# Optimization experiments

Measured on AMD Instinct MI355X. Metric: run time of the kernel, lower is better.

The kernel has to match this reference:

```python
import jax, jax.numpy as jnp
import numpy as np

B, T = 64, 2048
HID, FAST, SLOW, VOCAB = 256, 64, 256, 64
WRITE_THRESH = 0.4
NEG = -1000000000.0


def setup_inputs() -> dict:
    key = jax.random.key(0)
    ks = jax.random.split(key, 10)
    s = 0.05  # small init so gate sigmoids are not saturated
    return {
        "seq": jax.random.randint(ks[0], (B, T), 0, VOCAB),
        "emb": jax.random.normal(ks[1], (VOCAB, HID), jnp.float32),        # encoder embedding table
        "Wg": jax.random.normal(ks[2], (HID, 1), jnp.float32) * s,         # write_gate
        "bg": jnp.zeros((1,), jnp.float32),
        "Wd": jax.random.normal(ks[3], (HID, 1), jnp.float32) * s,         # demotion_net
        "bd": jnp.zeros((1,), jnp.float32),
        "Wq": jax.random.normal(ks[4], (HID, HID), jnp.float32) * s,       # read_head.q_proj
        "bq": jnp.zeros((HID,), jnp.float32),
        "Wo": jax.random.normal(ks[5], (HID, VOCAB), jnp.float32) * s,     # read_head.out
        "bo": jnp.zeros((VOCAB,), jnp.float32),
    }


def _process_sequence(h, Wg, bg, Wd, bd):
    # h: (B, T, H). Sequential LRU tiered-memory scatter, vectorized over batch.
    Bb, Tt, H = h.shape

    def step(state, tok_h):
        fm, sm, fa, sa, fu, su = state
        ws = jax.nn.sigmoid(tok_h @ Wg + bg)[:, 0]          # (B,) write score
        act = ws >= WRITE_THRESH                            # skip rows with score < 0.4
        fa = fa + fu.astype(jnp.int32)                      # age occupied slots
        sa = sa + su.astype(jnp.int32)
        free = ~fu
        has_free = jnp.any(free, axis=1)                    # (B,)
        free_idx = jnp.argmax(free, axis=1)                 # first free fast slot
        dem = ((fm @ Wd)[..., 0] + bd[0])                   # (B, FAST) demotion scores
        dem_slot = jnp.argmin(dem, axis=1)
        fslot = jnp.where(has_free, free_idx, dem_slot)     # fast slot to write
        foh = jax.nn.one_hot(fslot, FAST, dtype=bool)
        wf = act[:, None] & foh                              # (B, FAST) fast-write mask
        # value demoted to slow (only used when fast was full)
        demoted = jnp.take_along_axis(fm, fslot[:, None, None], axis=1)[:, 0, :]
        slow_act = act & ~has_free
        sfree = ~su
        s_has_free = jnp.any(sfree, axis=1)
        ss = jnp.where(s_has_free, jnp.argmax(sfree, axis=1), jnp.argmax(sa, axis=1))
        soh = jax.nn.one_hot(ss, SLOW, dtype=bool)
        wsm = slow_act[:, None] & soh                        # (B, SLOW) slow-write mask
        sm = jnp.where(wsm[..., None], demoted[:, None, :], sm)
        sa = jnp.where(wsm, 0, sa)
        su = su | wsm
        tok = jax.lax.stop_gradient(tok_h)                   # original writes tok_h.detach()
        fm = jnp.where(wf[..., None], tok[:, None, :], fm)
        fa = jnp.where(wf, 0, fa)
        fu = fu | wf
        return (fm, sm, fa, sa, fu, su), None

    init = (
        jnp.zeros((Bb, FAST, H), h.dtype),
        jnp.zeros((Bb, SLOW, H), h.dtype),
        jnp.zeros((Bb, FAST), jnp.int32),
        jnp.zeros((Bb, SLOW), jnp.int32),
        jnp.zeros((Bb, FAST), bool),
        jnp.zeros((Bb, SLOW), bool),
    )
    hs = jnp.swapaxes(h[:, : Tt - 3], 0, 1)                  # loop runs for T-3 tokens
    (fm, sm, fa, sa, fu, su), _ = jax.lax.scan(step, init, hs)
    memory = jnp.concatenate([fm, sm], axis=1)               # (B, F+S, H)
    mask = jnp.concatenate([fu, su], axis=1).astype(h.dtype)
    slow_mask = su.astype(h.dtype)
    return memory, mask, slow_mask


def reference(seq, emb, Wg, bg, Wd, bd, Wq, bq, Wo, bo):
    h = emb[seq]                                             # encoder: (B, T, H)
    memory, mask, slow_mask = _process_sequence(h, Wg, bg, Wd, bd)
    # ReadHead
    q = h[:, -1, :] @ Wq + bq                                # (B, H)
    scores = jnp.einsum("bnh,bh->bn", memory, q)
    scores = jnp.where(mask == 0, NEG, scores)
    attn = jax.nn.softmax(scores, axis=-1)
    ctx = jnp.einsum("bn,bnh->bh", attn, memory)
    logits = ctx @ Wo + bo                                   # (B, VOCAB)
    return logits, slow_mask
```

## Files before the change

kernel.cpp:

```cpp
#include <hip/hip_runtime.h>
#include <math.h>

#define BB 64
#define TT 2048
#define HIDD 256
#define FASTN 64
#define SLOWN 256
#define VOC 64
#define TLOOP (TT - 3)
#define NEGC -1000000000.0f
#define EPAD 257
#define NEGBIG (-(1 << 20))
#define BYTEAT(U, J) ((int)(((U) >> (8 * (J))) & 0xFFu))

__global__ __launch_bounds__(512) void k_one(
    const int* __restrict__ seq, const float* __restrict__ emb,
    const float* __restrict__ Wg, const float* __restrict__ bg,
    const float* __restrict__ Wd, const float* __restrict__ bd,
    const float* __restrict__ Wq, const float* __restrict__ bq,
    const float* __restrict__ Wo, const float* __restrict__ bo,
    float* __restrict__ out) {
  const int b = blockIdx.x;
  const int tid = threadIdx.x;
  const int lane = tid & 63;
  const int wv = tid >> 6;

  __shared__ float embS[VOC * EPAD];
  __shared__ __align__(16) unsigned char zsB[2080];
  __shared__ float qLastS[HIDD], ctxS[HIDD];
  __shared__ float pp[4][64];
  __shared__ float gp8[8][64], dp8[8][64];
  __shared__ float wS[64];
  __shared__ int prS[64], invS[64], cntTok[64];
  __shared__ int CS[4];
  __shared__ int PsS[4][64], QsS[4][64], aEndS[4][64], eSS[4][64];

  const int4* seq4 = (const int4*)(seq + b * TT);
  int4 sqa = make_int4(0, 0, 0, 0), sqb = make_int4(0, 0, 0, 0);
  if (tid < 256) { sqa = seq4[2 * tid]; sqb = seq4[2 * tid + 1]; }
  const int lastv = seq[b * TT + TT - 1];

  const float4* emb4 = (const float4*)emb;
  for (int i = tid; i < VOC * 64; i += 512) {
    float4 e = emb4[i];
    float* d = &embS[(i >> 6) * EPAD + ((i & 63) << 2)];
    d[0] = e.x; d[1] = e.y; d[2] = e.z; d[3] = e.w;
  }
  __syncthreads();

  {
    const int v = tid & 63, kp = tid >> 6;
    const float* er = &embS[v * EPAD + kp * 32];
    const float* wg = &Wg[kp * 32];
    const float* wd = &Wd[kp * 32];
    float g = 0.f, d = 0.f;
#pragma unroll 8
    for (int k = 0; k < 32; ++k) { float e = er[k]; g += e * wg[k]; d += e * wd[k]; }
    gp8[kp][v] = g; dp8[kp][v] = d;
  }
  __syncthreads();

  float qacc = 0.f;
  if (tid < 64) {
    float g = bg[0], dv = bd[0];
#pragma unroll
    for (int p = 0; p < 8; ++p) { g += gp8[p][tid]; dv += dp8[p][tid]; }
    int act = (1.f / (1.f + expf(-g)) >= 0.4f) ? 1 : 0;
    int r = 0;
#pragma unroll
    for (int s = 1; s < 64; ++s) {
      float du = __shfl_xor(dv, s);
      int u = lane ^ s;
      r += (du < dv || (du == dv && u < lane)) ? 1 : 0;
    }
    invS[r] = tid;
    prS[tid] = act ? r : 0xFF;
  } else if (tid >= 256) {
    const int j = tid - 256;
    const float* eL = &embS[lastv * EPAD];
#pragma unroll 8
    for (int k = 0; k < 128; ++k) qacc += eL[k] * Wq[k * HIDD + j];
  }
  __syncthreads();

  int by[8], cAct = 0, incl = 0;
  if (tid < 256) {
    const int t0 = tid * 8;
    int tk[8] = {sqa.x, sqa.y, sqa.z, sqa.w, sqb.x, sqb.y, sqb.z, sqb.w};
#pragma unroll
    for (int j = 0; j < 8; ++j) {
      int r = prS[tk[j]];
      by[j] = (t0 + j < TLOOP) ? r : 0xFF;
      cAct += (by[j] != 0xFF) ? 1 : 0;
    }
    incl = cAct;
    for (int s = 1; s < 64; s <<= 1) {
      int t = __shfl_up(incl, s);
      if (lane >= s) incl += t;
    }
    if (lane == 63) CS[wv] = incl;
  } else {
    const int j = tid - 256;
    const float* eL = &embS[lastv * EPAD];
#pragma unroll 8
    for (int k = 128; k < 256; ++k) qacc += eL[k] * Wq[k * HIDD + j];
    qLastS[j] = qacc + bq[j];
  }
  __syncthreads();

  const int A = CS[0] + CS[1] + CS[2] + CS[3];
  const int fsplit = A < 64 ? A : 64;
  const int nL = A - fsplit;
  const int win = nL < 256 ? nL : 256;
  const int wstart = A - win;
  const int L = (((A + 3) >> 2) + 15) & ~15;

  if (tid < 256) {
    int Ow = 0;
#pragma unroll
    for (int w2 = 0; w2 < 4; ++w2) Ow += (w2 < wv) ? CS[w2] : 0;
    int pos = Ow + incl - cAct;
#pragma unroll
    for (int j = 0; j < 8; ++j)
      if (by[j] != 0xFF) zsB[pos++] = (unsigned char)by[j];
  } else {
    const int j = tid - 256;
    out[BB * VOC + b * SLOWN + j] = (j < win) ? 1.0f : 0.0f;
  }
  __syncthreads();

  if (tid < 256) {
    const int baseW = wv * L;
    const int endW = min(baseW + L, A);
    int P = 0, Q = NEGBIG;
    for (int g = baseW; g < endW; g += 16) {
      uint4 t4 = *(const uint4*)(zsB + g);
      unsigned dsw[4] = {t4.x, t4.y, t4.z, t4.w};
      const int gHi = min(g + 16, endW);
      if (gHi == g + 16 && gHi <= fsplit) {
#pragma unroll
        for (int d = 0; d < 4; ++d)
#pragma unroll
          for (int j = 0; j < 4; ++j) {
            int x = (BYTEAT(dsw[d], j) <= lane) ? 1 : 0;
            P += x; Q += x;
          }
      } else if (gHi == g + 16 && g >= fsplit) {
#pragma unroll
        for (int d = 0; d < 4; ++d)
#pragma unroll
          for (int j = 0; j < 4; ++j) {
            int x = (BYTEAT(dsw[d], j) <= lane) ? 1 : 0;
            P += x - 1;
            Q = max(Q + x - 1, x);
          }
      } else {
#pragma unroll
        for (int d = 0; d < 4; ++d)
#pragma unroll
          for (int j = 0; j < 4; ++j) {
            int i = g + d * 4 + j;
            int x = (BYTEAT(dsw[d], j) <= lane) ? 1 : 0;
            bool vld = i < endW;
            bool fil = i < fsplit;
            int p = fil ? x : x - 1;
            int q = fil ? NEGBIG : x;
            int Pn = P + p;
            int Qn = max(Q + p, q);
            P = vld ? Pn : P;
            Q = vld ? Qn : Q;
          }
      }
    }
    PsS[wv][lane] = P;
    QsS[wv][lane] = Q;
  } else {
    const int v = tid & 63, part = wv - 4;
    const float* er = &embS[v * EPAD + part * 64];
    const float* qr = &qLastS[part * 64];
    float s = 0.f;
#pragma unroll 8
    for (int k = 0; k < 64; ++k) s += er[k] * qr[k];
    pp[part][v] = s;
  }
  __syncthreads();

  if (tid < 256) {
    int a = 0;
    for (int w2 = 0; w2 < wv; ++w2)
      a = max(a + PsS[w2][lane], QsS[w2][lane]);
    int e = 0;
    const int baseW = wv * L;
    const int endW = min(baseW + L, A);
    for (int g = baseW; g < endW; g += 16) {
      uint4 t4 = *(const uint4*)(zsB + g);
      unsigned dsw[4] = {t4.x, t4.y, t4.z, t4.w};
      const int gHi = min(g + 16, endW);
      const bool full = (gHi == g + 16);
      if (full && gHi <= fsplit) {
#pragma unroll
        for (int d = 0; d < 4; ++d)
#pragma unroll
          for (int j = 0; j < 4; ++j)
            a += (BYTEAT(dsw[d], j) <= lane) ? 1 : 0;
      } else if (full && g >= fsplit && gHi <= wstart) {
#pragma unroll
        for (int d = 0; d < 4; ++d)
#pragma unroll
          for (int j = 0; j < 4; ++j) {
            int xm1 = (BYTEAT(dsw[d], j) <= lane) ? 0 : -1;
            a = max(a, 1) + xm1;
          }
      } else if (full && g >= wstart) {
#pragma unroll
        for (int d = 0; d < 4; ++d)
#pragma unroll
          for (int j = 0; j < 4; ++j) {
            int xm1 = (BYTEAT(dsw[d], j) <= lane) ? 0 : -1;
            e += (a > 0) ? 1 : 0;
            a = max(a, 1) + xm1;
          }
      } else {
#pragma unroll
        for (int d = 0; d < 4; ++d)
#pragma unroll
          for (int j = 0; j < 4; ++j) {
            int i = g + d * 4 + j;
            int x = (BYTEAT(dsw[d], j) <= lane) ? 1 : 0;
            bool vld = i < endW;
            bool fil = i < fsplit;
            bool wg = vld && (i >= wstart);
            e += (wg && a > 0) ? 1 : 0;
            int af = a + x;
            int al = max(a, 1) + (x - 1);
            int an = fil ? af : al;
            a = vld ? an : a;
          }
      }
    }
    aEndS[wv][lane] = a;
    eSS[wv][lane] = e;
  }
  __syncthreads();

  if (tid < 64) {
    int af = aEndS[3][lane];
    int et = eSS[0][lane] + eSS[1][lane] + eSS[2][lane] + eSS[3][lane];
    int ap = __shfl_up(af, 1); if (lane == 0) ap = 0;
    int ep = __shfl_up(et, 1); if (lane == 0) ep = 0;
    cntTok[invS[lane]] = (af - ap) + (et - ep);
    float sc = pp[0][tid] + pp[1][tid] + pp[2][tid] + pp[3][tid];
    int cc = cntTok[tid];
    float m = (cc > 0) ? sc : NEGC;
    for (int off = 32; off; off >>= 1) m = fmaxf(m, __shfl_xor(m, off));
    float w = (cc > 0) ? (float)cc * expf(sc - m) : 0.f;
    float z = w;
    for (int off = 32; off; off >>= 1) z += __shfl_xor(z, off);
    z += (float)(FASTN + SLOWN - (fsplit + win)) * expf(NEGC - m);
    wS[tid] = w / z;
  }
  __syncthreads();

  if (tid < 256) {
    float cacc = 0.f;
#pragma unroll 8
    for (int u = 0; u < 64; ++u) cacc += wS[u] * embS[u * EPAD + tid];
    ctxS[tid] = cacc;
  }
  __syncthreads();

  if (tid < 256) {
    const int o = tid & 63, part = tid >> 6;
    const float* cr = &ctxS[part * 64];
    const float* wr = &Wo[part * 64 * VOC + o];
    float s = 0.f;
#pragma unroll 8
    for (int k = 0; k < 64; ++k) s += cr[k] * wr[k * VOC];
    pp[part][o] = s;
  }
  __syncthreads();
  if (tid < 64)
    out[b * VOC + tid] = pp[0][tid] + pp[1][tid] + pp[2][tid] + pp[3][tid] + bo[tid];
}

extern "C" void kernel_launch(void* const* d_in, const int* in_sizes, int n_in,
                              void* d_out, int out_size, void* d_ws, size_t ws_size,
                              hipStream_t stream) {
  const int*   seq = (const int*)d_in[0];
  const float* emb = (const float*)d_in[1];
  const float* Wg  = (const float*)d_in[2];
  const float* bg  = (const float*)d_in[3];
  const float* Wd  = (const float*)d_in[4];
  const float* bd  = (const float*)d_in[5];
  const float* Wq  = (const float*)d_in[6];
  const float* bq  = (const float*)d_in[7];
  const float* Wo  = (const float*)d_in[8];
  const float* bo  = (const float*)d_in[9];
  float* out = (float*)d_out;

  k_one<<<dim3(64), dim3(512), 0, stream>>>(seq, emb, Wg, bg, Wd, bd,
                                            Wq, bq, Wo, bo, out);
}
```

Before: 102.7 us.

## Split token scan across all eight waves and stage Wo in shared memory

The two-pass segmented prefix scan over compacted write tokens now uses all 8 wavefronts instead of 4, halving each wave's chunk length. The q-score dot products that used to run on the idle waves move into a separate phase after the scan, adding a barrier. Each 16-byte chunk of token bytes is loaded one iteration ahead to hide LDS latency. Wo is copied into shared memory up front so the final projection reads LDS instead of strided global memory. This adds 64KB of LDS and an extra sync, which may limit occupancy.

```diff
diff --git a/kernel.cpp b/kernel.cpp
--- a/kernel.cpp
+++ b/kernel.cpp
@@ -26,14 +26,15 @@
   const int wv = tid >> 6;
 
   __shared__ float embS[VOC * EPAD];
-  __shared__ __align__(16) unsigned char zsB[2080];
+  __shared__ float WoS[HIDD * VOC];
+  __shared__ __align__(16) unsigned char zsB[2304];
   __shared__ float qLastS[HIDD], ctxS[HIDD];
   __shared__ float pp[4][64];
   __shared__ float gp8[8][64], dp8[8][64];
   __shared__ float wS[64];
   __shared__ int prS[64], invS[64], cntTok[64];
   __shared__ int CS[4];
-  __shared__ int PsS[4][64], QsS[4][64], aEndS[4][64], eSS[4][64];
+  __shared__ int PsS[8][64], QsS[8][64], aEndS[8][64], eSS[8][64];
 
   const int4* seq4 = (const int4*)(seq + b * TT);
   int4 sqa = make_int4(0, 0, 0, 0), sqb = make_int4(0, 0, 0, 0);
@@ -45,6 +46,11 @@
     float4 e = emb4[i];
     float* d = &embS[(i >> 6) * EPAD + ((i & 63) << 2)];
     d[0] = e.x; d[1] = e.y; d[2] = e.z; d[3] = e.w;
+  }
+  {
+    const float4* Wo4 = (const float4*)Wo;
+    float4* WoS4 = (float4*)WoS;
+    for (int i = tid; i < HIDD * VOC / 4; i += 512) WoS4[i] = Wo4[i];
   }
   __syncthreads();
 
@@ -113,7 +119,7 @@
   const int nL = A - fsplit;
   const int win = nL < 256 ? nL : 256;
   const int wstart = A - win;
-  const int L = (((A + 3) >> 2) + 15) & ~15;
+  const int L = (((A + 7) >> 3) + 15) & ~15;
 
   if (tid < 256) {
     int Ow = 0;
@@ -129,13 +135,15 @@
   }
   __syncthreads();
 
-  if (tid < 256) {
-    const int baseW = wv * L;
-    const int endW = min(baseW + L, A);
+  const int baseW = wv * L;
+  const int endW = min(baseW + L, A);
+
+  {
     int P = 0, Q = NEGBIG;
+    uint4 cur = *(const uint4*)(zsB + baseW);
     for (int g = baseW; g < endW; g += 16) {
-      uint4 t4 = *(const uint4*)(zsB + g);
-      unsigned dsw[4] = {t4.x, t4.y, t4.z, t4.w};
+      uint4 nxt = *(const uint4*)(zsB + g + 16);
+      unsigned dsw[4] = {cur.x, cur.y, cur.z, cur.w};
       const int gHi = min(g + 16, endW);
       if (gHi == g + 16 && gHi <= fsplit) {
 #pragma unroll
@@ -171,30 +179,22 @@
             Q = vld ? Qn : Q;
           }
       }
+      cur = nxt;
     }
     PsS[wv][lane] = P;
     QsS[wv][lane] = Q;
-  } else {
-    const int v = tid & 63, part = wv - 4;
-    const float* er = &embS[v * EPAD + part * 64];
-    const float* qr = &qLastS[part * 64];
-    float s = 0.f;
-#pragma unroll 8
-    for (int k = 0; k < 64; ++k) s += er[k] * qr[k];
-    pp[part][v] = s;
-  }
-  __syncthreads();
-
-  if (tid < 256) {
+  }
+  __syncthreads();
+
+  {
     int a = 0;
     for (int w2 = 0; w2 < wv; ++w2)
       a = max(a + PsS[w2][lane], QsS[w2][lane]);
     int e = 0;
-    const int baseW = wv * L;
-    const int endW = min(baseW + L, A);
+    uint4 cur = *(const uint4*)(zsB + baseW);
     for (int g = baseW; g < endW; g += 16) {
-      uint4 t4 = *(const uint4*)(zsB + g);
-      unsigned dsw[4] = {t4.x, t4.y, t4.z, t4.w};
+      uint4 nxt = *(const uint4*)(zsB + g + 16);
+      unsigned dsw[4] = {cur.x, cur.y, cur.z, cur.w};
       const int gHi = min(g + 16, endW);
       const bool full = (gHi == g + 16);
       if (full && gHi <= fsplit) {
@@ -237,15 +237,29 @@
             a = vld ? an : a;
           }
       }
+      cur = nxt;
     }
     aEndS[wv][lane] = a;
     eSS[wv][lane] = e;
   }
   __syncthreads();
 
+  if (tid < 256) {
+    const int v = tid & 63, part = tid >> 6;
+    const float* er = &embS[v * EPAD + part * 64];
+    const float* qr = &qLastS[part * 64];
+    float s = 0.f;
+#pragma unroll 8
+    for (int k = 0; k < 64; ++k) s += er[k] * qr[k];
+    pp[part][v] = s;
+  }
+  __syncthreads();
+
   if (tid < 64) {
-    int af = aEndS[3][lane];
-    int et = eSS[0][lane] + eSS[1][lane] + eSS[2][lane] + eSS[3][lane];
+    int af = aEndS[7][lane];
+    int et = 0;
+#pragma unroll
+    for (int w2 = 0; w2 < 8; ++w2) et += eSS[w2][lane];
     int ap = __shfl_up(af, 1); if (lane == 0) ap = 0;
     int ep = __shfl_up(et, 1); if (lane == 0) ep = 0;
     cntTok[invS[lane]] = (af - ap) + (et - ep);
@@ -272,7 +286,7 @@
   if (tid < 256) {
     const int o = tid & 63, part = tid >> 6;
     const float* cr = &ctxS[part * 64];
-    const float* wr = &Wo[part * 64 * VOC + o];
+    const float* wr = &WoS[part * 64 * VOC + o];
     float s = 0.f;
 #pragma unroll 8
     for (int k = 0; k < 64; ++k) s += cr[k] * wr[k * VOC];
```

New measurement: 98.60 us. 4.0% less time.
